# Kernel tuning notes

Hardware: AMD Instinct MI355X
Metric: run time of the kernel (lower is better)

## Reference

```python
import jax, jax.numpy as jnp
import numpy as np

N_NODES = 100000
N_EDGES = 1600000
C = 128          # in_channels
H = 32           # hidden MLP width
D = 1            # Dirichlet concentration dims
T = 3            # Taylor params (estimate_bpr=True)
JITTER = 1e-20


def gcn_conv(x, W, b, edge_index, n_nodes):
    """PyG GCNConv: add self-loops, symmetric normalization, aggregate to target."""
    h = x @ W                                   # [N, C] transform first (smaller than gathering raw x then transforming per-edge)
    src = jnp.concatenate([edge_index[0], jnp.arange(n_nodes)])
    dst = jnp.concatenate([edge_index[1], jnp.arange(n_nodes)])
    deg = jax.ops.segment_sum(jnp.ones_like(dst, dtype=h.dtype), dst, num_segments=n_nodes)
    dinv = jnp.where(deg > 0, jax.lax.rsqrt(deg), 0.0)
    norm = dinv[src] * dinv[dst]                # [E+N]
    msg = h[src] * norm[:, None]                # gather + scale  [E+N, C]
    out = jax.ops.segment_sum(msg, dst, num_segments=n_nodes)  # scatter-add
    return out + b


def setup_inputs() -> dict:
    key = jax.random.key(0)
    ks = jax.random.split(key, 20)
    s = 1.0 / np.sqrt(C)
    sh = 1.0 / np.sqrt(H)
    x = jax.random.normal(ks[0], (N_NODES, C), dtype=jnp.float32)
    edge_index = jax.random.randint(ks[1], (2, N_EDGES), 0, N_NODES)
    p = {
        "x": x, "edge_index": edge_index,
        # actor params
        "a_conv_W": jax.random.uniform(ks[2], (C, C), jnp.float32, -s, s),
        "a_conv_b": jnp.zeros((C,), jnp.float32),
        "a_l1_W": jax.random.uniform(ks[3], (C, H), jnp.float32, -s, s),
        "a_l1_b": jax.random.uniform(ks[4], (H,), jnp.float32, -s, s),
        "a_l2_W": jax.random.uniform(ks[5], (H, H), jnp.float32, -sh, sh),
        "a_l2_b": jax.random.uniform(ks[6], (H,), jnp.float32, -sh, sh),
        "a_l3_W": jax.random.uniform(ks[7], (H, D + T), jnp.float32, -sh, sh),
        "a_l3_b": jax.random.uniform(ks[8], (D + T,), jnp.float32, -sh, sh),
        # critic params
        "c_conv_W": jax.random.uniform(ks[9], (C, C), jnp.float32, -s, s),
        "c_conv_b": jnp.zeros((C,), jnp.float32),
        "c_l1_W": jax.random.uniform(ks[10], (C, H), jnp.float32, -s, s),
        "c_l1_b": jax.random.uniform(ks[11], (H,), jnp.float32, -s, s),
        "c_l2_W": jax.random.uniform(ks[12], (H, H), jnp.float32, -sh, sh),
        "c_l2_b": jax.random.uniform(ks[13], (H,), jnp.float32, -sh, sh),
        "c_l3_W": jax.random.uniform(ks[14], (H, 1), jnp.float32, -sh, sh),
        "c_l3_b": jax.random.uniform(ks[15], (1,), jnp.float32, -sh, sh),
    }
    return p


def reference(x, edge_index,
              a_conv_W, a_conv_b, a_l1_W, a_l1_b, a_l2_W, a_l2_b, a_l3_W, a_l3_b,
              c_conv_W, c_conv_b, c_l1_W, c_l1_b, c_l2_W, c_l2_b, c_l3_W, c_l3_b):
    n = x.shape[0]
    # ---- actor (GNNActor.forward) ----
    a = jax.nn.relu(gcn_conv(x, a_conv_W, a_conv_b, edge_index, n)) + x   # residual
    a = jax.nn.relu(a @ a_l1_W + a_l1_b)
    a = jax.nn.relu(a @ a_l2_W + a_l2_b)
    a_out = a @ a_l3_W + a_l3_b                      # [N, D+T]
    concentration = jax.nn.softplus(a_out[:, :D]).reshape(-1) + JITTER
    taylor_params = jax.nn.softplus(a_out[:, D:]) + JITTER
    # ---- critic (GNNCritic.forward) ----
    c = jax.nn.relu(gcn_conv(x, c_conv_W, c_conv_b, edge_index, n)) + x
    c = jnp.sum(c, axis=0)                           # graph readout [C]
    c = jax.nn.relu(c @ c_l1_W + c_l1_b)
    c = jax.nn.relu(c @ c_l2_W + c_l2_b)
    value = c @ c_l3_W + c_l3_b                      # [1]
    return concentration, taylor_params, value
```

## Files before the change

### kernel.cpp

```cpp
#include <hip/hip_runtime.h>
#include <math.h>

#define CCH 128
#define HID 32
#define SLOTS 64
#define NBINS 391
#define BSHIFT 8
#define BCAP 4608

typedef __attribute__((ext_vector_type(8))) short bf16x8;
typedef __attribute__((ext_vector_type(4))) float f32x4;

__device__ __forceinline__ unsigned bf16pk(float a, float b) {
    unsigned ua = __builtin_bit_cast(unsigned, a);
    unsigned ub = __builtin_bit_cast(unsigned, b);
    ua = (ua + 0x7FFFu + ((ua >> 16) & 1u)) >> 16;
    ub = (ub + 0x7FFFu + ((ub >> 16) & 1u)) >> 16;
    return ua | (ub << 16);
}
__device__ __forceinline__ unsigned short bf16s(float a) {
    unsigned ua = __builtin_bit_cast(unsigned, a);
    ua = (ua + 0x7FFFu + ((ua >> 16) & 1u)) >> 16;
    return (unsigned short)ua;
}
__device__ __forceinline__ float bflo(unsigned v) {
    return __builtin_bit_cast(float, v << 16);
}
__device__ __forceinline__ float bfhi(unsigned v) {
    return __builtin_bit_cast(float, v & 0xFFFF0000u);
}

__global__ void k_zero(float* __restrict__ csum, int* __restrict__ binCnt) {
    int t = threadIdx.x;
    if (t < CCH) csum[t] = 0.f;
    for (int i = t; i < NBINS; i += 256) binCnt[i] = 0;
}

__global__ __launch_bounds__(256, 4)
void k_bin(const int* __restrict__ ei, int E,
           int* __restrict__ binCnt, unsigned* __restrict__ stage) {
    int t = threadIdx.x;
    __shared__ int lcnt[NBINS];
    __shared__ int lofs[NBINS];
    const int nchunk = (E + 2047) / 2048;
    for (int ch = blockIdx.x; ch < nchunk; ch += gridDim.x) {
        int base = ch * 2048;
        for (int i = t; i < NBINS; i += 256) lcnt[i] = 0;
        __syncthreads();
        unsigned pk[8]; int bin[8];
#pragma unroll
        for (int k = 0; k < 8; k++) {
            int e = base + k * 256 + t;
            if (e < E) {
                unsigned src = (unsigned)ei[e];
                unsigned dst = (unsigned)ei[E + e];
                bin[k] = dst >> BSHIFT;
                pk[k] = src | ((dst & 0xFFu) << 17);
                atomicAdd(&lcnt[bin[k]], 1);
            } else bin[k] = -1;
        }
        __syncthreads();
        for (int i = t; i < NBINS; i += 256) {
            int c = lcnt[i];
            lofs[i] = c ? atomicAdd(&binCnt[i], c) : 0;
        }
        __syncthreads();
#pragma unroll
        for (int k = 0; k < 8; k++) {
            if (bin[k] >= 0) {
                int pos = atomicAdd(&lofs[bin[k]], 1);
                if (pos < BCAP)
                    stage[(long)bin[k] * BCAP + pos] = pk[k];
            }
        }
        __syncthreads();
    }
}

__global__ __launch_bounds__(256)
void k_place(const unsigned* __restrict__ stage, const int* __restrict__ binCnt,
             int* __restrict__ cnt, int* __restrict__ csr) {
    __shared__ int lcnt[256];
    __shared__ int lofs[256];
    __shared__ int lcur[256];
    __shared__ int wtot[4];
    __shared__ unsigned ssrc[BCAP];
    __shared__ unsigned short sd8[BCAP];

    int t = threadIdx.x;
    int b = blockIdx.x;
    int count = binCnt[b];
    if (count > BCAP) count = BCAP;
    const unsigned* sp = stage + (long)b * BCAP;
    int dbase = b << BSHIFT;

    lcnt[t] = 0;
    __syncthreads();
    for (int i = t; i < count; i += 256)
        atomicAdd(&lcnt[sp[i] >> 17], 1);
    __syncthreads();

    int craw = lcnt[t];
    int cc = craw > SLOTS ? SLOTS : craw;
    int lane = t & 63, wv = t >> 6;
    int x = cc;
#pragma unroll
    for (int d = 1; d < 64; d <<= 1) {
        int y = __shfl_up(x, d, 64);
        if (lane >= d) x += y;
    }
    if (lane == 63) wtot[wv] = x;
    __syncthreads();
    int pre = 0;
#pragma unroll
    for (int k = 0; k < 4; k++) pre += (k < wv) ? wtot[k] : 0;
    int excl = pre + x - cc;
    lofs[t] = excl;
    lcur[t] = excl;
    int total = wtot[0] + wtot[1] + wtot[2] + wtot[3];
    __syncthreads();

    for (int i = t; i < count; i += 256) {
        unsigned p = sp[i];
        int d8 = (int)(p >> 17);
        int pos = atomicAdd(&lcur[d8], 1);
        if (pos - lofs[d8] < SLOTS) {
            ssrc[pos] = p & 0x1FFFFu;
            sd8[pos] = (unsigned short)d8;
        }
    }
    __syncthreads();

    for (int i = t; i < total; i += 256) {
        int d8 = sd8[i];
        csr[(long)(dbase + d8) * SLOTS + (i - lofs[d8])] = (int)ssrc[i];
    }
    cnt[dbase + t] = craw;
}

__global__ __launch_bounds__(256, 4)
void k_prep(const float* __restrict__ aW, const float* __restrict__ cW,
            const float* __restrict__ x, const int* __restrict__ cnt,
            unsigned short* __restrict__ Wt, unsigned short* __restrict__ xsb,
            float* __restrict__ csum, int N) {
    __shared__ float scs[CCH];
    int t = threadIdx.x;
    int id = blockIdx.x * 256 + t;
    if (id < 32768) {
        int conv = id >> 14;
        int rem = id & 16383;
        int n = rem >> 7;
        int k = rem & 127;
        const float* W = conv ? cW : aW;
        Wt[id] = bf16s(W[k * CCH + n]);
    }
    if (blockIdx.x == 0 && t < 64) ((unsigned*)xsb)[(long)N * 64 + t] = 0u;

    const int n4 = N * 32;
    float c0 = 0.f, c1 = 0.f, c2 = 0.f, c3 = 0.f;
    const float4* x4 = (const float4*)x;
    uint2* xo = (uint2*)xsb;
    int stride = gridDim.x * 256;
    for (int i = id; i < n4; i += stride) {
        int node = i >> 5;
        float dv = rsqrtf((float)cnt[node] + 1.0f);
        float4 v = x4[i];
        c0 += v.x; c1 += v.y; c2 += v.z; c3 += v.w;
        uint2 p;
        p.x = bf16pk(dv * v.x, dv * v.y);
        p.y = bf16pk(dv * v.z, dv * v.w);
        xo[i] = p;
    }
    if (t < CCH) scs[t] = 0.f;
    __syncthreads();
    int c4 = (t & 31) * 4;
    atomicAdd(&scs[c4 + 0], c0);
    atomicAdd(&scs[c4 + 1], c1);
    atomicAdd(&scs[c4 + 2], c2);
    atomicAdd(&scs[c4 + 3], c3);
    __syncthreads();
    if (t < CCH) atomicAdd(&csum[t], scs[t]);
}

__global__ __launch_bounds__(256, 4)
void k_gather_y(const unsigned short* __restrict__ xs,
                const int* __restrict__ cnt,
                const int* __restrict__ csr,
                unsigned short* __restrict__ yb, int N) {
    int t = threadIdx.x;
    int lane = t & 63;
    int wid = t >> 6;
    int half = lane >> 5;
    int hl = lane & 31;
    int wg = blockIdx.x * 4 + wid;
    int stride = gridDim.x * 4;
    const uint2* xu = (const uint2*)xs;
    uint2* yu = (uint2*)yb;
    int npairs = N >> 1;

    for (int p = wg; p < npairs; p += stride) {
        int nA = p * 2;
        int degr = cnt[nA + half];
        float dvd = rsqrtf((float)degr + 1.0f);
        int deg = degr > SLOTS ? SLOTS : degr;
        int degA = __builtin_amdgcn_readlane(deg, 0);
        int degB = __builtin_amdgcn_readlane(deg, 32);
        int dmax = degA > degB ? degA : degB;
        dmax = __builtin_amdgcn_readfirstlane(dmax);

        int idxl = csr[(long)nA * SLOTS + lane + (lane & 32)];
        if (hl >= deg) idxl = N;

        uint2 vs = xu[(long)nA * 32 + lane];
        float a0 = bflo(vs.x), a1 = bfhi(vs.x);
        float a2 = bflo(vs.y), a3 = bfhi(vs.y);

        int dm = dmax < 32 ? dmax : 32;
        int dm8 = (dm + 7) & ~7;
        for (int e = 0; e < dm8; e += 8) {
            uint2 v[8];
#pragma unroll
            for (int k = 0; k < 8; k++) {
                int iA = __builtin_amdgcn_readlane(idxl, e + k);
                int iB = __builtin_amdgcn_readlane(idxl, 32 + e + k);
                int sidx = half ? iB : iA;
                v[k] = xu[(long)sidx * 32 + hl];
            }
#pragma unroll
            for (int k = 0; k < 8; k++) {
                a0 += bflo(v[k].x); a1 += bfhi(v[k].x);
                a2 += bflo(v[k].y); a3 += bfhi(v[k].y);
            }
        }
        if (dmax > 32) {
            int idxh = csr[(long)nA * SLOTS + lane + (lane & 32) + 32];
            if (hl + 32 >= deg) idxh = N;
            int dx8 = (dmax + 7) & ~7;
            for (int e = 32; e < dx8; e += 8) {
                uint2 v[8];
#pragma unroll
                for (int k = 0; k < 8; k++) {
                    int iA = __builtin_amdgcn_readlane(idxh, e - 32 + k);
                    int iB = __builtin_amdgcn_readlane(idxh, e + k);
                    int sidx = half ? iB : iA;
                    v[k] = xu[(long)sidx * 32 + hl];
                }
#pragma unroll
                for (int k = 0; k < 8; k++) {
                    a0 += bflo(v[k].x); a1 += bfhi(v[k].x);
                    a2 += bflo(v[k].y); a3 += bfhi(v[k].y);
                }
            }
        }
        uint2 o;
        o.x = bf16pk(dvd * a0, dvd * a1);
        o.y = bf16pk(dvd * a2, dvd * a3);
        yu[(long)nA * 32 + lane] = o;
    }
}

__global__ __launch_bounds__(256, 4)
void k_gemm_y(const unsigned short* __restrict__ yb,
              const float* __restrict__ x,
              const unsigned short* __restrict__ Wt,
              const float* __restrict__ ab, const float* __restrict__ cb,
              unsigned short* __restrict__ a1b, float* __restrict__ csum,
              int N) {
    __shared__ unsigned short Ws[128 * 128];
    __shared__ float scs[CCH];
    int t = threadIdx.x;
    int row0 = blockIdx.x * 128;
    int wid = t >> 6, lane = t & 63;
    int m = lane & 15, quad = lane >> 4;
    int mrow0 = row0 + wid * 32;

    bf16x8 afr[2][4];
#pragma unroll
    for (int rt = 0; rt < 2; rt++) {
        int row = mrow0 + rt * 16 + m; if (row >= N) row = N - 1;
        const unsigned short* yr = yb + (long)row * CCH;
#pragma unroll
        for (int ks = 0; ks < 4; ks++)
            afr[rt][ks] = *(const bf16x8*)(yr + ks * 32 + quad * 8);
    }

    for (int conv = 0; conv < 2; conv++) {
        __syncthreads();
        const uint4* src = (const uint4*)(Wt + conv * 16384);
#pragma unroll
        for (int i = 0; i < 8; i++) {
            int id = i * 256 + t;
            int n = id >> 4, c = id & 15;
            uint4 v = src[id];
            *(uint4*)(Ws + n * 128 + ((c ^ (n & 15)) * 8)) = v;
        }
        if (conv == 1 && t < CCH) scs[t] = 0.f;
        __syncthreads();

#pragma unroll
        for (int nt = 0; nt < 8; nt++) {
            int n = nt * 16 + m;
            f32x4 ac0 = {0.f, 0.f, 0.f, 0.f};
            f32x4 ac1 = {0.f, 0.f, 0.f, 0.f};
#pragma unroll
            for (int ks = 0; ks < 4; ks++) {
                bf16x8 b = *(const bf16x8*)(Ws + n * 128 + (((ks * 4 + quad) ^ m) * 8));
                ac0 = __builtin_amdgcn_mfma_f32_16x16x32_bf16(afr[0][ks], b, ac0, 0, 0, 0);
                ac1 = __builtin_amdgcn_mfma_f32_16x16x32_bf16(afr[1][ks], b, ac1, 0, 0, 0);
            }
            float bias = conv ? cb[n] : ab[n];
            float part = 0.f;
#pragma unroll
            for (int h = 0; h < 2; h++) {
#pragma unroll
                for (int r = 0; r < 4; r++) {
                    int row = mrow0 + quad * 4 + r + h * 16;
                    float acv = h ? ac1[r] : ac0[r];
                    if (row < N) {
                        if (conv == 0) {
                            float xv = x[(long)row * CCH + n];
                            float v = fmaxf(acv + bias, 0.f) + xv;
                            a1b[(long)row * CCH + n] = bf16s(v);
                        } else {
                            part += fmaxf(acv + bias, 0.f);
                        }
                    }
                }
            }
            if (conv) atomicAdd(&scs[n], part);
        }
    }
    __syncthreads();
    if (t < CCH) atomicAdd(&csum[t], scs[t]);
}

__device__ __forceinline__ float softplus_f(float v) {
    return fmaxf(v, 0.f) + log1pf(expf(-fabsf(v)));
}

__global__ __launch_bounds__(256, 3)
void k_mlp(const unsigned short* __restrict__ a1b,
           const float* __restrict__ W1, const float* __restrict__ b1,
           const float* __restrict__ W2, const float* __restrict__ b2,
           const float* __restrict__ W3, const float* __restrict__ b3,
           const float* __restrict__ csum,
           const float* __restrict__ cW1, const float* __restrict__ cb1,
           const float* __restrict__ cW2, const float* __restrict__ cb2,
           const float* __restrict__ cW3, const float* __restrict__ cb3,
           float* __restrict__ out, int N) {
    __shared__ unsigned rowsW[64 * 65];
    __shared__ float h1L[64 * 33];
    __shared__ float h2L[64 * 33];
    int t = threadIdx.x;
    int l = t & 63;
    int w = t >> 6;
    long nbase = (long)blockIdx.x * 64;

    const uint4* ga = (const uint4*)(a1b + nbase * CCH);
#pragma unroll
    for (int i = 0; i < 4; i++) {
        int idx = i * 256 + t;
        int node = idx >> 4;
        int ch = idx & 15;
        uint4 v = make_uint4(0, 0, 0, 0);
        if (nbase + node < N) v = ga[node * 16 + ch];
        unsigned* dst = &rowsW[node * 65 + ch * 4];
        dst[0] = v.x; dst[1] = v.y; dst[2] = v.z; dst[3] = v.w;
    }
    __syncthreads();

    int j0 = __builtin_amdgcn_readfirstlane(w * 8);

    float h1[8];
#pragma unroll
    for (int j = 0; j < 8; j++) h1[j] = b1[j0 + j];
    for (int kp = 0; kp < 64; kp++) {
        unsigned v = rowsW[l * 65 + kp];
        float f0 = __builtin_bit_cast(float, v << 16);
        float f1 = __builtin_bit_cast(float, v & 0xFFFF0000u);
        const float* w0 = W1 + (2 * kp) * HID + j0;
        const float* w1 = W1 + (2 * kp + 1) * HID + j0;
#pragma unroll
        for (int j = 0; j < 8; j++)
            h1[j] = fmaf(f1, w1[j], fmaf(f0, w0[j], h1[j]));
    }
#pragma unroll
    for (int j = 0; j < 8; j++) h1L[l * 33 + j0 + j] = fmaxf(h1[j], 0.f);
    __syncthreads();

    float h2[8];
#pragma unroll
    for (int j = 0; j < 8; j++) h2[j] = b2[j0 + j];
    for (int k = 0; k < HID; k++) {
        float hv = h1L[l * 33 + k];
        const float* wr = W2 + k * HID + j0;
#pragma unroll
        for (int j = 0; j < 8; j++)
            h2[j] = fmaf(hv, wr[j], h2[j]);
    }
#pragma unroll
    for (int j = 0; j < 8; j++) h2L[l * 33 + j0 + j] = fmaxf(h2[j], 0.f);
    __syncthreads();

    if (w == 0) {
        long node = nbase + l;
        if (node < N) {
            float o[4] = {b3[0], b3[1], b3[2], b3[3]};
            for (int k = 0; k < HID; k++) {
                float hv = h2L[l * 33 + k];
#pragma unroll
                for (int m = 0; m < 4; m++)
                    o[m] = fmaf(hv, W3[k * 4 + m], o[m]);
            }
            out[node] = softplus_f(o[0]) + 1e-20f;
            float* ty = out + N;
            ty[node * 3 + 0] = softplus_f(o[1]) + 1e-20f;
            ty[node * 3 + 1] = softplus_f(o[2]) + 1e-20f;
            ty[node * 3 + 2] = softplus_f(o[3]) + 1e-20f;
        }
    }

    if (blockIdx.x == 0) {
        __syncthreads();
        float* cv  = h1L;
        float* hh1 = h2L;
        float* hh2 = h2L + 64;
        if (t < CCH) cv[t] = csum[t];
        __syncthreads();
        if (t < HID) {
            float a = cb1[t];
            for (int k = 0; k < CCH; k++) a = fmaf(cv[k], cW1[k * HID + t], a);
            hh1[t] = fmaxf(a, 0.f);
        }
        __syncthreads();
        if (t < HID) {
            float a = cb2[t];
            for (int k = 0; k < HID; k++) a = fmaf(hh1[k], cW2[k * HID + t], a);
            hh2[t] = fmaxf(a, 0.f);
        }
        __syncthreads();
        if (t == 0) {
            float a = cb3[0];
            for (int k = 0; k < HID; k++) a = fmaf(hh2[k], cW3[k], a);
            out[(long)4 * N] = a;
        }
    }
}

extern "C" void kernel_launch(void* const* d_in, const int* in_sizes, int n_in,
                              void* d_out, int out_size, void* d_ws, size_t ws_size,
                              hipStream_t stream) {
    const float* x   = (const float*)d_in[0];
    const int*   ei  = (const int*)d_in[1];
    const float* aW  = (const float*)d_in[2];
    const float* ab  = (const float*)d_in[3];
    const float* aW1 = (const float*)d_in[4];
    const float* ab1 = (const float*)d_in[5];
    const float* aW2 = (const float*)d_in[6];
    const float* ab2 = (const float*)d_in[7];
    const float* aW3 = (const float*)d_in[8];
    const float* ab3 = (const float*)d_in[9];
    const float* cW  = (const float*)d_in[10];
    const float* cb  = (const float*)d_in[11];
    const float* cW1 = (const float*)d_in[12];
    const float* cb1 = (const float*)d_in[13];
    const float* cW2 = (const float*)d_in[14];
    const float* cb2 = (const float*)d_in[15];
    const float* cW3 = (const float*)d_in[16];
    const float* cb3 = (const float*)d_in[17];
    float* out = (float*)d_out;

    const int N = in_sizes[0] / CCH;
    const int E = in_sizes[1] / 2;

    char* ws = (char*)d_ws;
    size_t off = 0;
    auto take = [&](size_t bytes) { void* p = ws + off; off += (bytes + 255) & ~(size_t)255; return p; };
    int*            cnt    = (int*)           take((size_t)NBINS * 256 * 4);
    int*            binCnt = (int*)           take(NBINS * 4);
    float*          csum   = (float*)         take(CCH * 4);
    unsigned short* Wt     = (unsigned short*)take(2 * 16384 * 2);
    int*            csr    = (int*)           take((size_t)N * SLOTS * 4);
    unsigned*       stage  = (unsigned*)      take((size_t)NBINS * BCAP * 4);
    unsigned short* xsb    = (unsigned short*)take((size_t)(N + 1) * CCH * 2);
    unsigned short* ybb    = (unsigned short*)take((size_t)N * CCH * 2);
    unsigned short* a1b    = (unsigned short*)take((size_t)N * CCH * 2);
    (void)ws_size;

    k_zero<<<1, 256, 0, stream>>>(csum, binCnt);
    k_bin<<<512, 256, 0, stream>>>(ei, E, binCnt, stage);
    k_place<<<NBINS, 256, 0, stream>>>(stage, binCnt, cnt, csr);

    k_prep<<<512, 256, 0, stream>>>(aW, cW, x, cnt, Wt, xsb, csum, N);

    k_gather_y<<<2048, 256, 0, stream>>>(xsb, cnt, csr, ybb, N);

    const int gblocks = (N + 127) / 128;
    k_gemm_y<<<gblocks, 256, 0, stream>>>(ybb, x, Wt, ab, cb, a1b, csum, N);

    k_mlp<<<(N + 63) / 64, 256, 0, stream>>>(a1b, aW1, ab1, aW2, ab2, aW3, ab3,
                                             csum, cW1, cb1, cW2, cb2, cW3, cb3,
                                             out, N);
}
```

Before: 334.3 us.

## Issue all 32 neighbor gathers at once with prescaled CSR offsets

The gather kernel now issues loads for all 32 low neighbor slots before accumulating, instead of batches of 8 bounded by the actual degree. This exposes more memory-level parallelism. CSR entries are pre-shifted by 5 so the row offset needs no 64-bit multiply. The high-half extraction skips masking and reads the raw word as float, which leaves the low bf16 bits as a small error. The cost is more registers and unconditional loads from the padding row for low-degree nodes.

```diff
diff --git a/kernel.cpp b/kernel.cpp
--- a/kernel.cpp
+++ b/kernel.cpp
@@ -125,7 +125,7 @@
         int d8 = (int)(p >> 17);
         int pos = atomicAdd(&lcur[d8], 1);
         if (pos - lofs[d8] < SLOTS) {
-            ssrc[pos] = p & 0x1FFFFu;
+            ssrc[pos] = (p & 0x1FFFFu) << 5;
             sd8[pos] = (unsigned short)d8;
         }
     }
@@ -197,6 +197,7 @@
     const uint2* xu = (const uint2*)xs;
     uint2* yu = (uint2*)yb;
     int npairs = N >> 1;
+    int zoff = N << 5;
 
     for (int p = wg; p < npairs; p += stride) {
         int nA = p * 2;
@@ -209,46 +210,48 @@
         dmax = __builtin_amdgcn_readfirstlane(dmax);
 
         int idxl = csr[(long)nA * SLOTS + lane + (lane & 32)];
-        if (hl >= deg) idxl = N;
+        if (hl >= deg) idxl = zoff;
 
         uint2 vs = xu[(long)nA * 32 + lane];
+
+        uint2 v[32];
+#pragma unroll
+        for (int e = 0; e < 32; e++) {
+            int iA = __builtin_amdgcn_readlane(idxl, e);
+            int iB = __builtin_amdgcn_readlane(idxl, 32 + e);
+            int boff = half ? iB : iA;
+            v[e] = xu[boff + hl];
+        }
+
         float a0 = bflo(vs.x), a1 = bfhi(vs.x);
         float a2 = bflo(vs.y), a3 = bfhi(vs.y);
-
-        int dm = dmax < 32 ? dmax : 32;
-        int dm8 = (dm + 7) & ~7;
-        for (int e = 0; e < dm8; e += 8) {
-            uint2 v[8];
-#pragma unroll
-            for (int k = 0; k < 8; k++) {
-                int iA = __builtin_amdgcn_readlane(idxl, e + k);
-                int iB = __builtin_amdgcn_readlane(idxl, 32 + e + k);
-                int sidx = half ? iB : iA;
-                v[k] = xu[(long)sidx * 32 + hl];
-            }
-#pragma unroll
-            for (int k = 0; k < 8; k++) {
-                a0 += bflo(v[k].x); a1 += bfhi(v[k].x);
-                a2 += bflo(v[k].y); a3 += bfhi(v[k].y);
-            }
-        }
+#pragma unroll
+        for (int e = 0; e < 32; e++) {
+            a0 += bflo(v[e].x);
+            a1 += __builtin_bit_cast(float, v[e].x);
+            a2 += bflo(v[e].y);
+            a3 += __builtin_bit_cast(float, v[e].y);
+        }
+
         if (dmax > 32) {
             int idxh = csr[(long)nA * SLOTS + lane + (lane & 32) + 32];
-            if (hl + 32 >= deg) idxh = N;
+            if (hl + 32 >= deg) idxh = zoff;
             int dx8 = (dmax + 7) & ~7;
             for (int e = 32; e < dx8; e += 8) {
-                uint2 v[8];
+                uint2 w[8];
 #pragma unroll
                 for (int k = 0; k < 8; k++) {
                     int iA = __builtin_amdgcn_readlane(idxh, e - 32 + k);
                     int iB = __builtin_amdgcn_readlane(idxh, e + k);
-                    int sidx = half ? iB : iA;
-                    v[k] = xu[(long)sidx * 32 + hl];
+                    int boff = half ? iB : iA;
+                    w[k] = xu[boff + hl];
                 }
 #pragma unroll
                 for (int k = 0; k < 8; k++) {
-                    a0 += bflo(v[k].x); a1 += bfhi(v[k].x);
-                    a2 += bflo(v[k].y); a3 += bfhi(v[k].y);
+                    a0 += bflo(w[k].x);
+                    a1 += __builtin_bit_cast(float, w[k].x);
+                    a2 += bflo(w[k].y);
+                    a3 += __builtin_bit_cast(float, w[k].y);
                 }
             }
         }
```

Measured after the change: 336.7 us. Within noise of the previous version (+0.7%).
